# Kernel tuning notes

Hardware: AMD Instinct MI355X
Metric: run time of the kernel (lower is better)

The kernel has to match this reference:

```python
import jax, jax.numpy as jnp
import numpy as np

SCALE = 4
KUP = 5


def conv2d(x, w, b, pad=0):
    # x: (B,C,H,W), w: (O,I,kh,kw)
    y = jax.lax.conv_general_dilated(x, w, (1, 1), [(pad, pad), (pad, pad)],
                                     dimension_numbers=('NCHW', 'OIHW', 'NCHW'))
    return y + b[None, :, None, None]


def unfold(x, k):
    # torch F.unfold equivalent: (B,C,H,W) -> (B,C,k*k,H,W), channel-major patch order
    p = jax.lax.conv_general_dilated_patches(x, (k, k), (1, 1), [(k // 2, k // 2), (k // 2, k // 2)])
    B, _, H, W = p.shape
    return p.reshape(B, -1, k * k, H, W)


def layernorm(x, g, b, eps=1e-5):
    m = jnp.mean(x, -1, keepdims=True)
    v = jnp.mean((x - m) ** 2, -1, keepdims=True)
    return (x - m) * jax.lax.rsqrt(v + eps) * g + b


def sim(q, k):
    # q: (B,sH,sW,E) high-res queries, k: (B,H,W,E) low-res keys
    B, H, W, C = k.shape
    s, ku = SCALE, KUP
    q6 = q.reshape(B, H, s, W, s, C)
    kunf = unfold(jnp.transpose(k, (0, 3, 1, 2)), ku)  # (B,E,ku^2,H,W)
    a = jnp.einsum('bhswtc,bcphw->bhswtp', q6, kunf)
    return a.reshape(B, s * H, s * W, ku * ku)


def atn(attn, x):
    # attn: (B,sH,sW,ku^2), x: (B,H,W,C) low-res values
    B, H, W, C = x.shape
    s, ku = SCALE, KUP
    a6 = attn.reshape(B, H, s, W, s, ku * ku)
    xunf = unfold(jnp.transpose(x, (0, 3, 1, 2)), ku)  # (B,C,ku^2,H,W)
    o = jnp.einsum('bhswtp,bcphw->bhswtc', a6, xunf)
    return o.reshape(B, s * H, s * W, C)


def setup_inputs() -> dict:
    key = jax.random.key(0)
    ks = jax.random.split(key, 40)
    B, C, H, W, yC, E = 2, 64, 128, 128, 3, 64
    sc = 0.05
    def n(i, shape):
        return jax.random.normal(ks[i], shape, jnp.float32) * sc
    return {
        'x': jax.random.normal(ks[0], (B, C, H, W), jnp.float32),
        'y': jax.random.normal(ks[1], (B, yC, H * SCALE, W * SCALE), jnp.float32),
        'gate_w': n(2, (C, C, 1, 1)), 'gate_b': n(3, (C,)),
        'pc1a_w': n(4, (16, yC + C, 1, 1)), 'pc1a_b': n(5, (16,)),
        'pc1b_w': n(6, (16, 16, 5, 5)), 'pc1b_b': n(7, (16,)),
        'spa1_w': n(8, (16, 16, 3, 3)), 'spa1_b': n(9, (16,)),
        'spa2_w': n(10, (16, 16, 3, 3)), 'spa2_b': n(11, (16,)),
        'frq1_w': n(12, (16, 16, 1, 1)), 'frq1_b': n(13, (16,)),
        'frq2_w': n(14, (16, 16, 1, 1)), 'frq2_b': n(15, (16,)),
        'cat_w': n(16, (8, 32, 1, 1)), 'cat_b': n(17, (8,)),
        'ca1_w': n(18, (2, 8, 1, 1)), 'ca1_b': n(19, (2,)),
        'ca2_w': n(20, (8, 2, 1, 1)), 'ca2_b': n(21, (8,)),
        'pc3_w': n(22, (C, 8, 1, 1)), 'pc3_b': n(23, (C,)),
        'lny_g': jnp.ones((C,), jnp.float32), 'lny_b': jnp.zeros((C,), jnp.float32),
        'lnx_g': jnp.ones((C,), jnp.float32), 'lnx_b': jnp.zeros((C,), jnp.float32),
        'q_w': n(24, (E, C)), 'q_b': n(25, (E,)),
        'k_w': n(26, (E, C)), 'k_b': n(27, (E,)),
    }


def reference(x, y, gate_w, gate_b, pc1a_w, pc1a_b, pc1b_w, pc1b_b,
              spa1_w, spa1_b, spa2_w, spa2_b, frq1_w, frq1_b, frq2_w, frq2_b,
              cat_w, cat_b, ca1_w, ca1_b, ca2_w, ca2_b, pc3_w, pc3_b,
              lny_g, lny_b, lnx_g, lnx_b, q_w, q_b, k_w, k_b):
    B, C, H, W = x.shape
    s = SCALE
    up_x = jax.image.resize(x, (B, C, H * s, W * s), 'cubic')
    gate = jax.nn.sigmoid(conv2d(up_x, gate_w, gate_b))
    # pan_conv1: 1x1 then 5x5
    f = conv2d(jnp.concatenate([y, up_x], 1), pc1a_w, pc1a_b)
    f = conv2d(f, pc1b_w, pc1b_b, pad=2)
    # DDNF: spatial branch (residual conv block stand-in) + frequency branch (1x1 stand-in), cat -> 8ch
    spa = f + conv2d(jax.nn.relu(conv2d(f, spa1_w, spa1_b, pad=1)), spa2_w, spa2_b, pad=1)
    frq = conv2d(jax.nn.relu(conv2d(f, frq1_w, frq1_b)), frq2_w, frq2_b)
    f = conv2d(jnp.concatenate([spa, frq], 1), cat_w, cat_b)
    # ChannelAttention(8, reduction=4): SE-style
    pooled = jnp.mean(f, (2, 3), keepdims=True)
    w = jax.nn.sigmoid(conv2d(jax.nn.relu(conv2d(pooled, ca1_w, ca1_b)), ca2_w, ca2_b))
    f = f * w
    enc = conv2d(f, pc3_w, pc3_b)  # (B,C,sH,sW)
    yb = jnp.transpose(enc, (0, 2, 3, 1))
    xb = jnp.transpose(x, (0, 2, 3, 1))
    yn = layernorm(yb, lny_g, lny_b)
    xn = layernorm(xb, lnx_g, lnx_b)
    q = yn @ q_w.T + q_b  # (B,sH,sW,E)
    k = xn @ k_w.T + k_b  # (B,H,W,E)
    attn = jax.nn.softmax(sim(q, k), axis=-1)
    sapa = jnp.transpose(atn(attn, xb), (0, 3, 1, 2))
    final = gate * sapa + (1.0 - gate) * enc
    return (final, sapa, enc)
```

## Files before the change

### kernel.cpp

```cpp
#include <hip/hip_runtime.h>
#include <hip/hip_bf16.h>
#include <math.h>


#define DEVFN static __device__ __forceinline__

DEVFN float keys_w(float d) {
    if (d < 1.f) return ((1.5f * d - 2.5f) * d) * d + 1.f;
    if (d < 2.f) return ((-0.5f * d + 2.5f) * d - 4.f) * d + 2.f;
    return 0.f;
}

DEVFN void bicubic_axis(int o, int n, int idx4[4], float w4[4]) {
    float f = (o + 0.5f) * 0.25f - 0.5f;
    float fb = floorf(f);
    int ib = (int)fb;
    float t = f - fb;
    float ws[4];
    ws[0] = keys_w(1.f + t);
    ws[1] = keys_w(t);
    ws[2] = keys_w(1.f - t);
    ws[3] = keys_w(2.f - t);
    float s = 0.f;
#pragma unroll
    for (int m = 0; m < 4; m++) {
        int ix = ib - 1 + m;
        if (ix < 0 || ix >= n) ws[m] = 0.f;
        s += ws[m];
        idx4[m] = min(max(ix, 0), n - 1);
    }
    float inv = 1.f / s;
#pragma unroll
    for (int m = 0; m < 4; m++) w4[m] = ws[m] * inv;
}

DEVFN float sigm(float v) { return 1.f / (1.f + __expf(-v)); }

DEVFN unsigned short f2bf(float f) {
    __hip_bfloat16 h = __float2bfloat16(f);
    unsigned short u;
    __builtin_memcpy(&u, &h, 2);
    return u;
}
DEVFN float bf2f(unsigned short u) {
    union { unsigned int i; float f; } z;
    z.i = ((unsigned int)u) << 16;
    return z.f;
}

__global__ __launch_bounds__(256) void k_low(const float* __restrict__ x,
                                             const float* __restrict__ gw, const float* __restrict__ gb,
                                             const float* __restrict__ pw,
                                             const float* __restrict__ lg, const float* __restrict__ lb,
                                             const float* __restrict__ kw, const float* __restrict__ kbias,
                                             float* __restrict__ kb, float* __restrict__ xb,
                                             float* __restrict__ glo, float* __restrict__ plo) {
    int idx = blockIdx.x * 256 + threadIdx.x;
    int w = idx & 127, h = (idx >> 7) & 127, b = idx >> 14;
    const float* xp = x + (size_t)b * 64 * 16384 + (h << 7) + w;
    float xv[64];
#pragma unroll
    for (int c = 0; c < 64; c++) xv[c] = xp[(size_t)c << 14];
    float4* xbp = (float4*)(xb + (size_t)idx * 64);
#pragma unroll
    for (int c4 = 0; c4 < 16; c4++)
        xbp[c4] = make_float4(xv[4 * c4], xv[4 * c4 + 1], xv[4 * c4 + 2], xv[4 * c4 + 3]);
    float4* gp = (float4*)(glo + (size_t)idx * 64);
#pragma unroll
    for (int e4 = 0; e4 < 16; e4++) {
        float r[4];
#pragma unroll
        for (int u = 0; u < 4; u++) {
            int e = e4 * 4 + u;
            float s = gb[e];
#pragma unroll
            for (int c = 0; c < 64; c++) s = fmaf(xv[c], gw[e * 64 + c], s);
            r[u] = s;
        }
        gp[e4] = make_float4(r[0], r[1], r[2], r[3]);
    }
    float4* pp = (float4*)(plo + (size_t)idx * 16);
#pragma unroll
    for (int e4 = 0; e4 < 4; e4++) {
        float r[4];
#pragma unroll
        for (int u = 0; u < 4; u++) {
            int e = e4 * 4 + u;
            float s = 0.f;
#pragma unroll
            for (int c = 0; c < 64; c++) s = fmaf(xv[c], pw[e * 67 + 3 + c], s);
            r[u] = s;
        }
        pp[e4] = make_float4(r[0], r[1], r[2], r[3]);
    }
    float m = 0.f;
#pragma unroll
    for (int c = 0; c < 64; c++) m += xv[c];
    m *= (1.f / 64.f);
    float var = 0.f;
#pragma unroll
    for (int c = 0; c < 64; c++) {
        float d = xv[c] - m;
        var = fmaf(d, d, var);
    }
    var *= (1.f / 64.f);
    float rstd = rsqrtf(var + 1e-5f);
#pragma unroll
    for (int c = 0; c < 64; c++) xv[c] = (xv[c] - m) * rstd * lg[c] + lb[c];
    float4* kp = (float4*)(kb + (size_t)idx * 64);
#pragma unroll
    for (int e4 = 0; e4 < 16; e4++) {
        float r[4];
#pragma unroll
        for (int u = 0; u < 4; u++) {
            int e = e4 * 4 + u;
            float s = kbias[e];
#pragma unroll
            for (int c = 0; c < 64; c++) s = fmaf(xv[c], kw[e * 64 + c], s);
            r[u] = s;
        }
        kp[e4] = make_float4(r[0], r[1], r[2], r[3]);
    }
}

__global__ __launch_bounds__(256) void k_gp(const float* __restrict__ glo, const float* __restrict__ plo,
                                            const float* __restrict__ y,
                                            const float* __restrict__ paw, const float* __restrict__ pab,
                                            __hip_bfloat16* __restrict__ gate, float* __restrict__ f0) {
    __shared__ float v[68 * 81];
    int bid = blockIdx.x;
    int b = bid >> 10, i = (bid >> 1) & 511, j0 = (bid & 1) << 8;
    int t = threadIdx.x;
    int iy[4];
    float wy[4];
    bicubic_axis(i, 128, iy, wy);
    int c0 = (j0 >> 2) - 2;
    for (int e = t; e < 68 * 80; e += 256) {
        int ch = e % 80, lc = e / 80;
        int gc = c0 + lc;
        float val = 0.f;
        if ((unsigned)gc < 128u) {
            if (ch < 64) {
                val = wy[0] * glo[(size_t)((b * 128 + iy[0]) * 128 + gc) * 64 + ch] +
                      wy[1] * glo[(size_t)((b * 128 + iy[1]) * 128 + gc) * 64 + ch] +
                      wy[2] * glo[(size_t)((b * 128 + iy[2]) * 128 + gc) * 64 + ch] +
                      wy[3] * glo[(size_t)((b * 128 + iy[3]) * 128 + gc) * 64 + ch];
            } else {
                int cc = ch - 64;
                val = wy[0] * plo[(size_t)((b * 128 + iy[0]) * 128 + gc) * 16 + cc] +
                      wy[1] * plo[(size_t)((b * 128 + iy[1]) * 128 + gc) * 16 + cc] +
                      wy[2] * plo[(size_t)((b * 128 + iy[2]) * 128 + gc) * 16 + cc] +
                      wy[3] * plo[(size_t)((b * 128 + iy[3]) * 128 + gc) * 16 + cc];
            }
        }
        v[lc * 81 + ch] = val;
    }
    __syncthreads();
    int j = j0 + t;
    int jx[4];
    float wx[4];
    bicubic_axis(j, 128, jx, wx);
    int lx0 = jx[0] - c0, lx1 = jx[1] - c0, lx2 = jx[2] - c0, lx3 = jx[3] - c0;
    float out[80];
#pragma unroll
    for (int ch = 0; ch < 80; ch++)
        out[ch] = wx[0] * v[lx0 * 81 + ch] + wx[1] * v[lx1 * 81 + ch] +
                  wx[2] * v[lx2 * 81 + ch] + wx[3] * v[lx3 * 81 + ch];
    size_t pxoff = ((size_t)b << 18) + ((size_t)i << 9) + j;
    unsigned int uu[32];
#pragma unroll
    for (int k = 0; k < 32; k++) {
        unsigned short h0 = f2bf(sigm(out[2 * k]));
        unsigned short h1 = f2bf(sigm(out[2 * k + 1]));
        uu[k] = (unsigned int)h0 | ((unsigned int)h1 << 16);
    }
    uint4* gp4 = (uint4*)((unsigned short*)gate + pxoff * 64);
#pragma unroll
    for (int k4 = 0; k4 < 8; k4++)
        gp4[k4] = make_uint4(uu[4 * k4], uu[4 * k4 + 1], uu[4 * k4 + 2], uu[4 * k4 + 3]);
    float yc0 = y[((size_t)(b * 3 + 0) << 18) + ((size_t)i << 9) + j];
    float yc1 = y[((size_t)(b * 3 + 1) << 18) + ((size_t)i << 9) + j];
    float yc2 = y[((size_t)(b * 3 + 2) << 18) + ((size_t)i << 9) + j];
    float4* fp = (float4*)(f0 + pxoff * 16);
#pragma unroll
    for (int e4 = 0; e4 < 4; e4++) {
        float r[4];
#pragma unroll
        for (int u = 0; u < 4; u++) {
            int oc = e4 * 4 + u;
            r[u] = out[64 + oc] + pab[oc] + yc0 * paw[oc * 67 + 0] + yc1 * paw[oc * 67 + 1] + yc2 * paw[oc * 67 + 2];
        }
        fp[e4] = make_float4(r[0], r[1], r[2], r[3]);
    }
}

__global__ __launch_bounds__(256) void k_conv5(const float* __restrict__ fin,
                                               const float* __restrict__ w,
                                               const float* __restrict__ bias,
                                               float* __restrict__ fout) {
    int idx = blockIdx.x * 256 + threadIdx.x;
    int j = idx & 511, i = (idx >> 9) & 511, b = idx >> 18;
    float acc[16];
#pragma unroll
    for (int oc = 0; oc < 16; oc++) acc[oc] = bias[oc];
    for (int ky = 0; ky < 5; ky++) {
        int iy = i + ky - 2;
        if ((unsigned)iy >= 512u) continue;
        for (int kx = 0; kx < 5; kx++) {
            int jx = j + kx - 2;
            if ((unsigned)jx >= 512u) continue;
            const float4* fp = (const float4*)(fin + (((size_t)b << 18) + ((size_t)iy << 9) + jx) * 16);
            float vv[16];
            *(float4*)(vv + 0) = fp[0];
            *(float4*)(vv + 4) = fp[1];
            *(float4*)(vv + 8) = fp[2];
            *(float4*)(vv + 12) = fp[3];
            int kidx = ky * 5 + kx;
#pragma unroll
            for (int ic = 0; ic < 16; ic++) {
#pragma unroll
                for (int oc = 0; oc < 16; oc++)
                    acc[oc] = fmaf(vv[ic], w[(oc * 16 + ic) * 25 + kidx], acc[oc]);
            }
        }
    }
    float4* op = (float4*)(fout + (size_t)idx * 16);
#pragma unroll
    for (int e4 = 0; e4 < 4; e4++)
        op[e4] = make_float4(acc[4 * e4], acc[4 * e4 + 1], acc[4 * e4 + 2], acc[4 * e4 + 3]);
}

__global__ __launch_bounds__(256) void k_conv3r(const float* __restrict__ fin,
                                                const float* __restrict__ w,
                                                const float* __restrict__ bias,
                                                float* __restrict__ fout) {
    int idx = blockIdx.x * 256 + threadIdx.x;
    int j = idx & 511, i = (idx >> 9) & 511, b = idx >> 18;
    float acc[16];
#pragma unroll
    for (int oc = 0; oc < 16; oc++) acc[oc] = bias[oc];
#pragma unroll
    for (int ky = 0; ky < 3; ky++) {
        int iy = i + ky - 1;
        if ((unsigned)iy >= 512u) continue;
#pragma unroll
        for (int kx = 0; kx < 3; kx++) {
            int jx = j + kx - 1;
            if ((unsigned)jx >= 512u) continue;
            const float4* fp = (const float4*)(fin + (((size_t)b << 18) + ((size_t)iy << 9) + jx) * 16);
            float vv[16];
            *(float4*)(vv + 0) = fp[0];
            *(float4*)(vv + 4) = fp[1];
            *(float4*)(vv + 8) = fp[2];
            *(float4*)(vv + 12) = fp[3];
            int kidx = ky * 3 + kx;
#pragma unroll
            for (int ic = 0; ic < 16; ic++) {
#pragma unroll
                for (int oc = 0; oc < 16; oc++)
                    acc[oc] = fmaf(vv[ic], w[(oc * 16 + ic) * 9 + kidx], acc[oc]);
            }
        }
    }
    float4* op = (float4*)(fout + (size_t)idx * 16);
#pragma unroll
    for (int e4 = 0; e4 < 4; e4++)
        op[e4] = make_float4(fmaxf(acc[4 * e4], 0.f), fmaxf(acc[4 * e4 + 1], 0.f),
                             fmaxf(acc[4 * e4 + 2], 0.f), fmaxf(acc[4 * e4 + 3], 0.f));
}

__global__ __launch_bounds__(256) void k_tail(const float* __restrict__ f1,
                                              const float* __restrict__ t,
                                              const float* __restrict__ s2w, const float* __restrict__ s2b,
                                              const float* __restrict__ q1w, const float* __restrict__ q1b,
                                              const float* __restrict__ q2w, const float* __restrict__ q2b,
                                              const float* __restrict__ cw_, const float* __restrict__ cb_,
                                              float* __restrict__ f8) {
    int idx = blockIdx.x * 256 + threadIdx.x;
    int j = idx & 511, i = (idx >> 9) & 511, b = idx >> 18;
    float sp[16];
#pragma unroll
    for (int oc = 0; oc < 16; oc++) sp[oc] = s2b[oc];
#pragma unroll
    for (int ky = 0; ky < 3; ky++) {
        int iy = i + ky - 1;
        if ((unsigned)iy >= 512u) continue;
#pragma unroll
        for (int kx = 0; kx < 3; kx++) {
            int jx = j + kx - 1;
            if ((unsigned)jx >= 512u) continue;
            const float4* fp = (const float4*)(t + (((size_t)b << 18) + ((size_t)iy << 9) + jx) * 16);
            float vv[16];
            *(float4*)(vv + 0) = fp[0];
            *(float4*)(vv + 4) = fp[1];
            *(float4*)(vv + 8) = fp[2];
            *(float4*)(vv + 12) = fp[3];
            int kidx = ky * 3 + kx;
#pragma unroll
            for (int ic = 0; ic < 16; ic++) {
#pragma unroll
                for (int oc = 0; oc < 16; oc++)
                    sp[oc] = fmaf(vv[ic], s2w[(oc * 16 + ic) * 9 + kidx], sp[oc]);
            }
        }
    }
    float fv[16];
    const float4* f1p = (const float4*)(f1 + (size_t)idx * 16);
    *(float4*)(fv + 0) = f1p[0];
    *(float4*)(fv + 4) = f1p[1];
    *(float4*)(fv + 8) = f1p[2];
    *(float4*)(fv + 12) = f1p[3];
#pragma unroll
    for (int c = 0; c < 16; c++) sp[c] += fv[c];
    float mid[16];
#pragma unroll
    for (int r = 0; r < 16; r++) {
        float m = q1b[r];
#pragma unroll
        for (int c = 0; c < 16; c++) m = fmaf(fv[c], q1w[r * 16 + c], m);
        mid[r] = fmaxf(m, 0.f);
    }
    float fo[16];
#pragma unroll
    for (int r = 0; r < 16; r++) {
        float m = q2b[r];
#pragma unroll
        for (int c = 0; c < 16; c++) m = fmaf(mid[c], q2w[r * 16 + c], m);
        fo[r] = m;
    }
    float r8[8];
#pragma unroll
    for (int o = 0; o < 8; o++) {
        float a = cb_[o];
#pragma unroll
        for (int c = 0; c < 16; c++) a = fmaf(sp[c], cw_[o * 32 + c], a);
#pragma unroll
        for (int c = 0; c < 16; c++) a = fmaf(fo[c], cw_[o * 32 + 16 + c], a);
        r8[o] = a;
    }
    float4* op = (float4*)(f8 + (size_t)idx * 8);
    op[0] = make_float4(r8[0], r8[1], r8[2], r8[3]);
    op[1] = make_float4(r8[4], r8[5], r8[6], r8[7]);
}

__global__ __launch_bounds__(256) void k_pool(const float* __restrict__ f8, float* __restrict__ partials) {
    int b = blockIdx.x >> 4, blk = blockIdx.x & 15;
    const float4* fp = (const float4*)(f8 + (((size_t)b) << 18) * 8);
    float acc[8];
#pragma unroll
    for (int c = 0; c < 8; c++) acc[c] = 0.f;
    int p0 = blk * 16384;
    for (int p = p0 + threadIdx.x; p < p0 + 16384; p += 256) {
        float4 a0 = fp[p * 2], a1 = fp[p * 2 + 1];
        acc[0] += a0.x; acc[1] += a0.y; acc[2] += a0.z; acc[3] += a0.w;
        acc[4] += a1.x; acc[5] += a1.y; acc[6] += a1.z; acc[7] += a1.w;
    }
#pragma unroll
    for (int off = 32; off; off >>= 1) {
#pragma unroll
        for (int c = 0; c < 8; c++) acc[c] += __shfl_down(acc[c], off, 64);
    }
    __shared__ float ls[4][8];
    int lane = threadIdx.x & 63, wv = threadIdx.x >> 6;
    if (lane == 0) {
#pragma unroll
        for (int c = 0; c < 8; c++) ls[wv][c] = acc[c];
    }
    __syncthreads();
    if (threadIdx.x < 8) {
        float s = ls[0][threadIdx.x] + ls[1][threadIdx.x] + ls[2][threadIdx.x] + ls[3][threadIdx.x];
        partials[(b * 8 + threadIdx.x) * 16 + blk] = s;
    }
}

__global__ void k_se(const float* __restrict__ partials,
                     const float* __restrict__ w1, const float* __restrict__ b1,
                     const float* __restrict__ w2, const float* __restrict__ b2,
                     float* __restrict__ cw) {
    int b = threadIdx.x;
    if (b >= 2) return;
    float pooled[8];
#pragma unroll
    for (int c = 0; c < 8; c++) {
        float s = 0.f;
#pragma unroll
        for (int k = 0; k < 16; k++) s += partials[(b * 8 + c) * 16 + k];
        pooled[c] = s * (1.f / 262144.f);
    }
    float mid[2];
#pragma unroll
    for (int r = 0; r < 2; r++) {
        float m = b1[r];
#pragma unroll
        for (int c = 0; c < 8; c++) m = fmaf(w1[r * 8 + c], pooled[c], m);
        mid[r] = fmaxf(m, 0.f);
    }
#pragma unroll
    for (int c = 0; c < 8; c++) {
        float v = b2[c] + w2[c * 2 + 0] * mid[0] + w2[c * 2 + 1] * mid[1];
        cw[b * 8 + c] = 1.f / (1.f + __expf(-v));
    }
}

__global__ __launch_bounds__(256) void k_pc3(const float* __restrict__ f8, const float* __restrict__ cw,
                                             const float* __restrict__ w, const float* __restrict__ bias,
                                             const float* __restrict__ lg, const float* __restrict__ lb,
                                             const float* __restrict__ qw, const float* __restrict__ qbias,
                                             float* __restrict__ enc, unsigned short* __restrict__ qbuf) {
    int idx = blockIdx.x * 256 + threadIdx.x;
    int b = idx >> 18;
    size_t hi = (size_t)idx & 262143;
    const float4* fp = (const float4*)(f8 + (size_t)idx * 8);
    float4 a0 = fp[0], a1 = fp[1];
    float v[8] = {a0.x, a0.y, a0.z, a0.w, a1.x, a1.y, a1.z, a1.w};
#pragma unroll
    for (int c = 0; c < 8; c++) v[c] *= cw[b * 8 + c];
    float yn[64];
#pragma unroll
    for (int oc = 0; oc < 64; oc++) {
        float a = bias[oc];
#pragma unroll
        for (int c = 0; c < 8; c++) a = fmaf(v[c], w[oc * 8 + c], a);
        yn[oc] = a;
        enc[((size_t)(b * 64 + oc) << 18) + hi] = a;
    }
    float m = 0.f;
#pragma unroll
    for (int c = 0; c < 64; c++) m += yn[c];
    m *= (1.f / 64.f);
    float var = 0.f;
#pragma unroll
    for (int c = 0; c < 64; c++) {
        float d = yn[c] - m;
        var = fmaf(d, d, var);
    }
    var *= (1.f / 64.f);
    float rstd = rsqrtf(var + 1e-5f);
#pragma unroll
    for (int c = 0; c < 64; c++) yn[c] = (yn[c] - m) * rstd * lg[c] + lb[c];
    unsigned short* qp = qbuf + (size_t)idx * 64;
    for (int e0 = 0; e0 < 64; e0 += 8) {
        float qv[8];
#pragma unroll
        for (int u = 0; u < 8; u++) {
            float s = qbias[e0 + u];
#pragma unroll
            for (int c = 0; c < 64; c++) s = fmaf(yn[c], qw[(e0 + u) * 64 + c], s);
            qv[u] = s;
        }
        unsigned int pk[4];
#pragma unroll
        for (int u = 0; u < 4; u++)
            pk[u] = (unsigned int)f2bf(qv[2 * u]) | ((unsigned int)f2bf(qv[2 * u + 1]) << 16);
        *(uint4*)(qp + e0) = make_uint4(pk[0], pk[1], pk[2], pk[3]);
    }
}

__global__ __launch_bounds__(256) void k_attn(const float* __restrict__ enc,
                                              const __hip_bfloat16* __restrict__ gate,
                                              const unsigned short* __restrict__ qb,
                                              const float* __restrict__ kb, const float* __restrict__ xbv,
                                              float* __restrict__ sapa, float* __restrict__ fin) {
    __shared__ float tile[100 * 68];
    int tid = threadIdx.x;
    int bid = blockIdx.x;
    int b = bid >> 12, i = (bid >> 3) & 511, jb = bid & 7;
    int j0 = jb << 6;
    int h = i >> 2;
    int wbase = j0 >> 2;
    int cg = tid & 3, px = tid >> 2;
    int j = j0 + px;
    size_t pix = ((size_t)b << 18) + ((size_t)i << 9) + j;
    const uint4* qp = (const uint4*)(qb + pix * 64 + cg * 16);
    uint4 q0 = qp[0], q1 = qp[1];
    unsigned int qu[8] = {q0.x, q0.y, q0.z, q0.w, q1.x, q1.y, q1.z, q1.w};
    float q[16];
#pragma unroll
    for (int k = 0; k < 8; k++) {
        q[2 * k] = bf2f((unsigned short)(qu[k] & 0xffff));
        q[2 * k + 1] = bf2f((unsigned short)(qu[k] >> 16));
    }
    for (int s = tid; s < 1600; s += 256) {
        int p = s >> 4, e4 = s & 15;
        int row = p / 20, col = p - row * 20;
        int hh = h - 2 + row, ww = wbase - 2 + col;
        float4 val = make_float4(0.f, 0.f, 0.f, 0.f);
        if ((unsigned)hh < 128u && (unsigned)ww < 128u)
            val = ((const float4*)(kb + (size_t)((b * 128 + hh) * 128 + ww) * 64))[e4];
        *(float4*)(tile + p * 68 + e4 * 4) = val;
    }
    __syncthreads();
    int wl = px >> 2;
    float a[25];
#pragma unroll
    for (int dy = 0; dy < 5; dy++) {
#pragma unroll
        for (int dx = 0; dx < 5; dx++) {
            int lp = dy * 20 + wl + dx;
            const float4* kp = (const float4*)(tile + lp * 68 + cg * 16);
            float s = 0.f;
#pragma unroll
            for (int e4 = 0; e4 < 4; e4++) {
                float4 kv = kp[e4];
                s = fmaf(q[4 * e4 + 0], kv.x, s);
                s = fmaf(q[4 * e4 + 1], kv.y, s);
                s = fmaf(q[4 * e4 + 2], kv.z, s);
                s = fmaf(q[4 * e4 + 3], kv.w, s);
            }
            a[dy * 5 + dx] = s;
        }
    }
#pragma unroll
    for (int p = 0; p < 25; p++) {
        a[p] += __shfl_xor(a[p], 1, 4);
        a[p] += __shfl_xor(a[p], 2, 4);
    }
    float mx = a[0];
#pragma unroll
    for (int p = 1; p < 25; p++) mx = fmaxf(mx, a[p]);
    float Z = 0.f;
#pragma unroll
    for (int p = 0; p < 25; p++) {
        a[p] = __expf(a[p] - mx);
        Z += a[p];
    }
    float invZ = 1.f / Z;
    __syncthreads();
    for (int s = tid; s < 1600; s += 256) {
        int p = s >> 4, e4 = s & 15;
        int row = p / 20, col = p - row * 20;
        int hh = h - 2 + row, ww = wbase - 2 + col;
        float4 val = make_float4(0.f, 0.f, 0.f, 0.f);
        if ((unsigned)hh < 128u && (unsigned)ww < 128u)
            val = ((const float4*)(xbv + (size_t)((b * 128 + hh) * 128 + ww) * 64))[e4];
        *(float4*)(tile + p * 68 + e4 * 4) = val;
    }
    __syncthreads();
    float o[16];
#pragma unroll
    for (int k = 0; k < 16; k++) o[k] = 0.f;
#pragma unroll
    for (int dy = 0; dy < 5; dy++) {
#pragma unroll
        for (int dx = 0; dx < 5; dx++) {
            float wp = a[dy * 5 + dx];
            int lp = dy * 20 + wl + dx;
            const float4* xp = (const float4*)(tile + lp * 68 + cg * 16);
#pragma unroll
            for (int e4 = 0; e4 < 4; e4++) {
                float4 xv = xp[e4];
                o[4 * e4 + 0] = fmaf(wp, xv.x, o[4 * e4 + 0]);
                o[4 * e4 + 1] = fmaf(wp, xv.y, o[4 * e4 + 1]);
                o[4 * e4 + 2] = fmaf(wp, xv.z, o[4 * e4 + 2]);
                o[4 * e4 + 3] = fmaf(wp, xv.w, o[4 * e4 + 3]);
            }
        }
    }
    const uint4* gp4 = (const uint4*)((const unsigned short*)gate + pix * 64 + cg * 16);
    uint4 g0 = gp4[0], g1 = gp4[1];
    unsigned int gu[8] = {g0.x, g0.y, g0.z, g0.w, g1.x, g1.y, g1.z, g1.w};
    size_t obase = ((size_t)b << 24) + ((size_t)i << 9) + j;
    const float* ep = enc + obase;
#pragma unroll
    for (int cc = 0; cc < 16; cc++) {
        int c = cg * 16 + cc;
        size_t oidx = obase + ((size_t)c << 18);
        float sv = o[cc] * invZ;
        sapa[oidx] = sv;
        unsigned int wbits = gu[cc >> 1];
        unsigned short hb = (cc & 1) ? (unsigned short)(wbits >> 16) : (unsigned short)(wbits & 0xffff);
        float gv = bf2f(hb);
        float ev = ep[(size_t)c << 18];
        fin[oidx] = gv * sv + (1.f - gv) * ev;
    }
}

extern "C" void kernel_launch(void* const* d_in, const int* in_sizes, int n_in,
                              void* d_out, int out_size, void* d_ws, size_t ws_size,
                              hipStream_t stream) {
    const float* x = (const float*)d_in[0];
    const float* y = (const float*)d_in[1];
    const float* gate_w = (const float*)d_in[2];
    const float* gate_b = (const float*)d_in[3];
    const float* pc1a_w = (const float*)d_in[4];
    const float* pc1a_b = (const float*)d_in[5];
    const float* pc1b_w = (const float*)d_in[6];
    const float* pc1b_b = (const float*)d_in[7];
    const float* spa1_w = (const float*)d_in[8];
    const float* spa1_b = (const float*)d_in[9];
    const float* spa2_w = (const float*)d_in[10];
    const float* spa2_b = (const float*)d_in[11];
    const float* frq1_w = (const float*)d_in[12];
    const float* frq1_b = (const float*)d_in[13];
    const float* frq2_w = (const float*)d_in[14];
    const float* frq2_b = (const float*)d_in[15];
    const float* cat_w = (const float*)d_in[16];
    const float* cat_b = (const float*)d_in[17];
    const float* ca1_w = (const float*)d_in[18];
    const float* ca1_b = (const float*)d_in[19];
    const float* ca2_w = (const float*)d_in[20];
    const float* ca2_b = (const float*)d_in[21];
    const float* pc3_w = (const float*)d_in[22];
    const float* pc3_b = (const float*)d_in[23];
    const float* lny_g = (const float*)d_in[24];
    const float* lny_b = (const float*)d_in[25];
    const float* lnx_g = (const float*)d_in[26];
    const float* lnx_b = (const float*)d_in[27];
    const float* q_w = (const float*)d_in[28];
    const float* q_b = (const float*)d_in[29];
    const float* k_w = (const float*)d_in[30];
    const float* k_b = (const float*)d_in[31];

    float* out = (float*)d_out;
    float* finalp = out;
    float* sapap = out + 33554432;
    float* encp = out + 67108864;

    char* ws = (char*)d_ws;
    __hip_bfloat16* gate = (__hip_bfloat16*)ws;
    float* f0 = (float*)(ws + 67108864);
    float* f1 = (float*)(ws + 100663296);
    float* f8 = (float*)(ws + 134217728);
    float* kbuf = (float*)(ws + 150994944);
    float* xbuf = (float*)(ws + 159383552);
    float* partials = (float*)(ws + 167772160);
    float* cw = (float*)(ws + 167773184);
    float* glo = f1;
    float* plo = f1 + 2097152;
    float* tbuf = f0;
    unsigned short* qbuf = (unsigned short*)(ws + 67108864);

    dim3 blk(256);
    dim3 gridHi(2048);

    k_low<<<dim3(128), blk, 0, stream>>>(x, gate_w, gate_b, pc1a_w, lnx_g, lnx_b, k_w, k_b,
                                         kbuf, xbuf, glo, plo);
    k_gp<<<gridHi, blk, 0, stream>>>(glo, plo, y, pc1a_w, pc1a_b, gate, f0);
    k_conv5<<<gridHi, blk, 0, stream>>>(f0, pc1b_w, pc1b_b, f1);
    k_conv3r<<<gridHi, blk, 0, stream>>>(f1, spa1_w, spa1_b, tbuf);
    k_tail<<<gridHi, blk, 0, stream>>>(f1, tbuf, spa2_w, spa2_b, frq1_w, frq1_b,
                                       frq2_w, frq2_b, cat_w, cat_b, f8);
    k_pool<<<dim3(32), blk, 0, stream>>>(f8, partials);
    k_se<<<dim3(1), dim3(64), 0, stream>>>(partials, ca1_w, ca1_b, ca2_w, ca2_b, cw);
    k_pc3<<<gridHi, blk, 0, stream>>>(f8, cw, pc3_w, pc3_b, lny_g, lny_b, q_w, q_b, encp, qbuf);
    k_attn<<<dim3(8192), blk, 0, stream>>>(encp, gate, qbuf, kbuf, xbuf, sapap, finalp);
}
```

Before: 946.5 us.

## Reuse conv input rows across wavefront lanes via shuffles in stencil kernels

The 5x5, 3x3 and tail conv kernels now assign each 64-lane wavefront a 60-column row segment. Each lane loads one 16-channel pixel per filter row, and the remaining horizontal taps are obtained from neighbour lanes with shuffles instead of separate global loads. This cuts redundant global/L1 loads by roughly the kernel width, at the cost of many shuffle instructions and a few idle halo lanes. Launch grids are resized to cover 9 segments per row.

Result: slower. 1.270 ms (+34.2%).

```diff
diff --git a/kernel.cpp b/kernel.cpp
--- a/kernel.cpp
+++ b/kernel.cpp
@@ -198,75 +198,118 @@
                                                const float* __restrict__ w,
                                                const float* __restrict__ bias,
                                                float* __restrict__ fout) {
-    int idx = blockIdx.x * 256 + threadIdx.x;
-    int j = idx & 511, i = (idx >> 9) & 511, b = idx >> 18;
+    int W = blockIdx.x * 4 + (threadIdx.x >> 6);
+    int lane = threadIdx.x & 63;
+    int seg = W % 9;
+    int rw = W / 9;
+    int i = rw & 511, b = rw >> 9;
+    int j0 = seg * 60;
+    int colL = j0 + lane - 2;
+    bool colOK = (unsigned)colL < 512u;
     float acc[16];
 #pragma unroll
     for (int oc = 0; oc < 16; oc++) acc[oc] = bias[oc];
     for (int ky = 0; ky < 5; ky++) {
         int iy = i + ky - 2;
-        if ((unsigned)iy >= 512u) continue;
-        for (int kx = 0; kx < 5; kx++) {
-            int jx = j + kx - 2;
-            if ((unsigned)jx >= 512u) continue;
-            const float4* fp = (const float4*)(fin + (((size_t)b << 18) + ((size_t)iy << 9) + jx) * 16);
-            float vv[16];
-            *(float4*)(vv + 0) = fp[0];
-            *(float4*)(vv + 4) = fp[1];
-            *(float4*)(vv + 8) = fp[2];
-            *(float4*)(vv + 12) = fp[3];
-            int kidx = ky * 5 + kx;
+        float t0[16];
+        if ((unsigned)iy < 512u && colOK) {
+            const float4* p = (const float4*)(fin + (((size_t)b << 18) + ((size_t)iy << 9) + colL) * 16);
+            *(float4*)(t0 + 0) = p[0];
+            *(float4*)(t0 + 4) = p[1];
+            *(float4*)(t0 + 8) = p[2];
+            *(float4*)(t0 + 12) = p[3];
+        } else {
+#pragma unroll
+            for (int ic = 0; ic < 16; ic++) t0[ic] = 0.f;
+        }
+#pragma unroll
+        for (int ic = 0; ic < 16; ic++) {
+            float v = t0[ic];
+#pragma unroll
+            for (int oc = 0; oc < 16; oc++)
+                acc[oc] = fmaf(v, w[(oc * 16 + ic) * 25 + ky * 5 + 0], acc[oc]);
+        }
+#pragma unroll
+        for (int dx = 1; dx < 5; dx++) {
+            float tv[16];
+#pragma unroll
+            for (int ic = 0; ic < 16; ic++) tv[ic] = __shfl(t0[ic], lane + dx, 64);
 #pragma unroll
             for (int ic = 0; ic < 16; ic++) {
+                float v = tv[ic];
 #pragma unroll
                 for (int oc = 0; oc < 16; oc++)
-                    acc[oc] = fmaf(vv[ic], w[(oc * 16 + ic) * 25 + kidx], acc[oc]);
+                    acc[oc] = fmaf(v, w[(oc * 16 + ic) * 25 + ky * 5 + dx], acc[oc]);
             }
         }
     }
-    float4* op = (float4*)(fout + (size_t)idx * 16);
-#pragma unroll
-    for (int e4 = 0; e4 < 4; e4++)
-        op[e4] = make_float4(acc[4 * e4], acc[4 * e4 + 1], acc[4 * e4 + 2], acc[4 * e4 + 3]);
+    int j = j0 + lane;
+    if (lane < 60 && j < 512) {
+        float4* op = (float4*)(fout + (((size_t)b << 18) + ((size_t)i << 9) + j) * 16);
+        op[0] = make_float4(acc[0], acc[1], acc[2], acc[3]);
+        op[1] = make_float4(acc[4], acc[5], acc[6], acc[7]);
+        op[2] = make_float4(acc[8], acc[9], acc[10], acc[11]);
+        op[3] = make_float4(acc[12], acc[13], acc[14], acc[15]);
+    }
 }
 
 __global__ __launch_bounds__(256) void k_conv3r(const float* __restrict__ fin,
                                                 const float* __restrict__ w,
                                                 const float* __restrict__ bias,
                                                 float* __restrict__ fout) {
-    int idx = blockIdx.x * 256 + threadIdx.x;
-    int j = idx & 511, i = (idx >> 9) & 511, b = idx >> 18;
+    int W = blockIdx.x * 4 + (threadIdx.x >> 6);
+    int lane = threadIdx.x & 63;
+    int seg = W % 9;
+    int rw = W / 9;
+    int i = rw & 511, b = rw >> 9;
+    int j0 = seg * 60;
+    int colL = j0 + lane - 1;
+    bool colOK = (unsigned)colL < 512u;
     float acc[16];
 #pragma unroll
     for (int oc = 0; oc < 16; oc++) acc[oc] = bias[oc];
-#pragma unroll
     for (int ky = 0; ky < 3; ky++) {
         int iy = i + ky - 1;
-        if ((unsigned)iy >= 512u) continue;
-#pragma unroll
-        for (int kx = 0; kx < 3; kx++) {
-            int jx = j + kx - 1;
-            if ((unsigned)jx >= 512u) continue;
-            const float4* fp = (const float4*)(fin + (((size_t)b << 18) + ((size_t)iy << 9) + jx) * 16);
-            float vv[16];
-            *(float4*)(vv + 0) = fp[0];
-            *(float4*)(vv + 4) = fp[1];
-            *(float4*)(vv + 8) = fp[2];
-            *(float4*)(vv + 12) = fp[3];
-            int kidx = ky * 3 + kx;
+        float t0[16];
+        if ((unsigned)iy < 512u && colOK) {
+            const float4* p = (const float4*)(fin + (((size_t)b << 18) + ((size_t)iy << 9) + colL) * 16);
+            *(float4*)(t0 + 0) = p[0];
+            *(float4*)(t0 + 4) = p[1];
+            *(float4*)(t0 + 8) = p[2];
+            *(float4*)(t0 + 12) = p[3];
+        } else {
+#pragma unroll
+            for (int ic = 0; ic < 16; ic++) t0[ic] = 0.f;
+        }
+#pragma unroll
+        for (int ic = 0; ic < 16; ic++) {
+            float v = t0[ic];
+#pragma unroll
+            for (int oc = 0; oc < 16; oc++)
+                acc[oc] = fmaf(v, w[(oc * 16 + ic) * 9 + ky * 3 + 0], acc[oc]);
+        }
+#pragma unroll
+        for (int dx = 1; dx < 3; dx++) {
+            float tv[16];
+#pragma unroll
+            for (int ic = 0; ic < 16; ic++) tv[ic] = __shfl(t0[ic], lane + dx, 64);
 #pragma unroll
             for (int ic = 0; ic < 16; ic++) {
+                float v = tv[ic];
 #pragma unroll
                 for (int oc = 0; oc < 16; oc++)
-                    acc[oc] = fmaf(vv[ic], w[(oc * 16 + ic) * 9 + kidx], acc[oc]);
+                    acc[oc] = fmaf(v, w[(oc * 16 + ic) * 9 + ky * 3 + dx], acc[oc]);
             }
         }
     }
-    float4* op = (float4*)(fout + (size_t)idx * 16);
-#pragma unroll
-    for (int e4 = 0; e4 < 4; e4++)
-        op[e4] = make_float4(fmaxf(acc[4 * e4], 0.f), fmaxf(acc[4 * e4 + 1], 0.f),
-                             fmaxf(acc[4 * e4 + 2], 0.f), fmaxf(acc[4 * e4 + 3], 0.f));
+    int j = j0 + lane;
+    if (lane < 60 && j < 512) {
+        float4* op = (float4*)(fout + (((size_t)b << 18) + ((size_t)i << 9) + j) * 16);
+        op[0] = make_float4(fmaxf(acc[0], 0.f), fmaxf(acc[1], 0.f), fmaxf(acc[2], 0.f), fmaxf(acc[3], 0.f));
+        op[1] = make_float4(fmaxf(acc[4], 0.f), fmaxf(acc[5], 0.f), fmaxf(acc[6], 0.f), fmaxf(acc[7], 0.f));
+        op[2] = make_float4(fmaxf(acc[8], 0.f), fmaxf(acc[9], 0.f), fmaxf(acc[10], 0.f), fmaxf(acc[11], 0.f));
+        op[3] = make_float4(fmaxf(acc[12], 0.f), fmaxf(acc[13], 0.f), fmaxf(acc[14], 0.f), fmaxf(acc[15], 0.f));
+    }
 }
 
 __global__ __launch_bounds__(256) void k_tail(const float* __restrict__ f1,
@@ -276,40 +319,64 @@
                                               const float* __restrict__ q2w, const float* __restrict__ q2b,
                                               const float* __restrict__ cw_, const float* __restrict__ cb_,
                                               float* __restrict__ f8) {
-    int idx = blockIdx.x * 256 + threadIdx.x;
-    int j = idx & 511, i = (idx >> 9) & 511, b = idx >> 18;
+    int W = blockIdx.x * 4 + (threadIdx.x >> 6);
+    int lane = threadIdx.x & 63;
+    int seg = W % 9;
+    int rw = W / 9;
+    int i = rw & 511, b = rw >> 9;
+    int j0 = seg * 60;
+    int colL = j0 + lane - 1;
+    bool colOK = (unsigned)colL < 512u;
+    int j = j0 + lane;
+    bool outOK = (lane < 60) && (j < 512);
     float sp[16];
 #pragma unroll
     for (int oc = 0; oc < 16; oc++) sp[oc] = s2b[oc];
-#pragma unroll
     for (int ky = 0; ky < 3; ky++) {
         int iy = i + ky - 1;
-        if ((unsigned)iy >= 512u) continue;
-#pragma unroll
-        for (int kx = 0; kx < 3; kx++) {
-            int jx = j + kx - 1;
-            if ((unsigned)jx >= 512u) continue;
-            const float4* fp = (const float4*)(t + (((size_t)b << 18) + ((size_t)iy << 9) + jx) * 16);
-            float vv[16];
-            *(float4*)(vv + 0) = fp[0];
-            *(float4*)(vv + 4) = fp[1];
-            *(float4*)(vv + 8) = fp[2];
-            *(float4*)(vv + 12) = fp[3];
-            int kidx = ky * 3 + kx;
+        float t0[16];
+        if ((unsigned)iy < 512u && colOK) {
+            const float4* p = (const float4*)(t + (((size_t)b << 18) + ((size_t)iy << 9) + colL) * 16);
+            *(float4*)(t0 + 0) = p[0];
+            *(float4*)(t0 + 4) = p[1];
+            *(float4*)(t0 + 8) = p[2];
+            *(float4*)(t0 + 12) = p[3];
+        } else {
+#pragma unroll
+            for (int ic = 0; ic < 16; ic++) t0[ic] = 0.f;
+        }
+#pragma unroll
+        for (int ic = 0; ic < 16; ic++) {
+            float v = t0[ic];
+#pragma unroll
+            for (int oc = 0; oc < 16; oc++)
+                sp[oc] = fmaf(v, s2w[(oc * 16 + ic) * 9 + ky * 3 + 0], sp[oc]);
+        }
+#pragma unroll
+        for (int dx = 1; dx < 3; dx++) {
+            float tv[16];
+#pragma unroll
+            for (int ic = 0; ic < 16; ic++) tv[ic] = __shfl(t0[ic], lane + dx, 64);
 #pragma unroll
             for (int ic = 0; ic < 16; ic++) {
+                float v = tv[ic];
 #pragma unroll
                 for (int oc = 0; oc < 16; oc++)
-                    sp[oc] = fmaf(vv[ic], s2w[(oc * 16 + ic) * 9 + kidx], sp[oc]);
+                    sp[oc] = fmaf(v, s2w[(oc * 16 + ic) * 9 + ky * 3 + dx], sp[oc]);
             }
         }
     }
     float fv[16];
-    const float4* f1p = (const float4*)(f1 + (size_t)idx * 16);
-    *(float4*)(fv + 0) = f1p[0];
-    *(float4*)(fv + 4) = f1p[1];
-    *(float4*)(fv + 8) = f1p[2];
-    *(float4*)(fv + 12) = f1p[3];
+    if (outOK) {
+        const float4* f1p = (const float4*)(f1 + (((size_t)b << 18) + ((size_t)i << 9) + j) * 16);
+        *(float4*)(fv + 0) = f1p[0];
+        *(float4*)(fv + 4) = f1p[1];
+        *(float4*)(fv + 8) = f1p[2];
+        *(float4*)(fv + 12) = f1p[3];
+    } else {
+#pragma unroll
+        for (int c = 0; c < 16; c++) fv[c] = 0.f;
+    }
 #pragma unroll
     for (int c = 0; c < 16; c++) sp[c] += fv[c];
     float mid[16];
@@ -338,9 +405,11 @@
         for (int c = 0; c < 16; c++) a = fmaf(fo[c], cw_[o * 32 + 16 + c], a);
         r8[o] = a;
     }
-    float4* op = (float4*)(f8 + (size_t)idx * 8);
-    op[0] = make_float4(r8[0], r8[1], r8[2], r8[3]);
-    op[1] = make_float4(r8[4], r8[5], r8[6], r8[7]);
+    if (outOK) {
+        float4* op = (float4*)(f8 + (((size_t)b << 18) + ((size_t)i << 9) + j) * 8);
+        op[0] = make_float4(r8[0], r8[1], r8[2], r8[3]);
+        op[1] = make_float4(r8[4], r8[5], r8[6], r8[7]);
+    }
 }
 
 __global__ __launch_bounds__(256) void k_pool(const float* __restrict__ f8, float* __restrict__ partials) {
@@ -632,14 +701,15 @@
 
     dim3 blk(256);
     dim3 gridHi(2048);
+    dim3 gridWave(2304);
 
     k_low<<<dim3(128), blk, 0, stream>>>(x, gate_w, gate_b, pc1a_w, lnx_g, lnx_b, k_w, k_b,
                                          kbuf, xbuf, glo, plo);
     k_gp<<<gridHi, blk, 0, stream>>>(glo, plo, y, pc1a_w, pc1a_b, gate, f0);
-    k_conv5<<<gridHi, blk, 0, stream>>>(f0, pc1b_w, pc1b_b, f1);
-    k_conv3r<<<gridHi, blk, 0, stream>>>(f1, spa1_w, spa1_b, tbuf);
-    k_tail<<<gridHi, blk, 0, stream>>>(f1, tbuf, spa2_w, spa2_b, frq1_w, frq1_b,
-                                       frq2_w, frq2_b, cat_w, cat_b, f8);
+    k_conv5<<<gridWave, blk, 0, stream>>>(f0, pc1b_w, pc1b_b, f1);
+    k_conv3r<<<gridWave, blk, 0, stream>>>(f1, spa1_w, spa1_b, tbuf);
+    k_tail<<<gridWave, blk, 0, stream>>>(f1, tbuf, spa2_w, spa2_b, frq1_w, frq1_b,
+                                         frq2_w, frq2_b, cat_w, cat_b, f8);
     k_pool<<<dim3(32), blk, 0, stream>>>(f8, partials);
     k_se<<<dim3(1), dim3(64), 0, stream>>>(partials, ca1_w, ca1_b, ca2_w, ca2_b, cw);
     k_pc3<<<gridHi, blk, 0, stream>>>(f8, cw, pc3_w, pc3_b, lny_g, lny_b, q_w, q_b, encp, qbuf);
```

## Stage conv input halos in LDS and pre-transpose conv weights

Applied to the files above, without the earlier changes.

The 5x5 and 3x3 high-res convolution kernels now load a 4x64-pixel tile plus halo into shared memory once per block (padded stride of 20 floats per pixel), then read neighbour taps from LDS instead of global memory. A small prep kernel transposes the conv weights to tap-major, oc-contiguous layout so the inner FMA loop reads weights contiguously (uniform scalar loads). Boundary checks move into the tile fill. This adds an extra launch and LDS pressure that could lower occupancy.

After: 846.7 us. 10.5% less time.

```diff
diff --git a/kernel.cpp b/kernel.cpp
--- a/kernel.cpp
+++ b/kernel.cpp
@@ -46,6 +46,24 @@
     union { unsigned int i; float f; } z;
     z.i = ((unsigned int)u) << 16;
     return z.f;
+}
+
+__global__ __launch_bounds__(256) void k_prep(const float* __restrict__ w5,
+                                              const float* __restrict__ w3a,
+                                              const float* __restrict__ w3b,
+                                              float* __restrict__ wT5,
+                                              float* __restrict__ wT3a,
+                                              float* __restrict__ wT3b) {
+    int t = blockIdx.x * 256 + threadIdx.x;
+    if (t < 6400) {
+        int tap = t >> 8, ic = (t >> 4) & 15, oc = t & 15;
+        wT5[t] = w5[(oc * 16 + ic) * 25 + tap];
+    }
+    if (t < 2304) {
+        int tap = t >> 8, ic = (t >> 4) & 15, oc = t & 15;
+        wT3a[t] = w3a[(oc * 16 + ic) * 9 + tap];
+        wT3b[t] = w3b[(oc * 16 + ic) * 9 + tap];
+    }
 }
 
 __global__ __launch_bounds__(256) void k_low(const float* __restrict__ x,
@@ -195,117 +213,157 @@
 }
 
 __global__ __launch_bounds__(256) void k_conv5(const float* __restrict__ fin,
-                                               const float* __restrict__ w,
+                                               const float* __restrict__ wT,
                                                const float* __restrict__ bias,
                                                float* __restrict__ fout) {
-    int idx = blockIdx.x * 256 + threadIdx.x;
-    int j = idx & 511, i = (idx >> 9) & 511, b = idx >> 18;
+    __shared__ float lds[8 * 68 * 20];
+    int tid = threadIdx.x;
+    int bid = blockIdx.x;
+    int seg = bid & 7, it = (bid >> 3) & 127, b = bid >> 10;
+    int i0 = it * 4, j0 = seg * 64;
+    for (int s = tid; s < 2176; s += 256) {
+        int part = s & 3, px = s >> 2;
+        int row = px / 68, col = px - row * 68;
+        int gi = i0 - 2 + row, gj = j0 - 2 + col;
+        float4 v = make_float4(0.f, 0.f, 0.f, 0.f);
+        if ((unsigned)gi < 512u && (unsigned)gj < 512u)
+            v = *(const float4*)(fin + (((size_t)b << 18) + ((size_t)gi << 9) + gj) * 16 + part * 4);
+        *(float4*)(&lds[(row * 68 + col) * 20 + part * 4]) = v;
+    }
+    __syncthreads();
+    int tx = tid & 63, ty = tid >> 6;
     float acc[16];
 #pragma unroll
     for (int oc = 0; oc < 16; oc++) acc[oc] = bias[oc];
+#pragma unroll
     for (int ky = 0; ky < 5; ky++) {
-        int iy = i + ky - 2;
-        if ((unsigned)iy >= 512u) continue;
+#pragma unroll
         for (int kx = 0; kx < 5; kx++) {
-            int jx = j + kx - 2;
-            if ((unsigned)jx >= 512u) continue;
-            const float4* fp = (const float4*)(fin + (((size_t)b << 18) + ((size_t)iy << 9) + jx) * 16);
+            const float* p = &lds[((ty + ky) * 68 + tx + kx) * 20];
             float vv[16];
-            *(float4*)(vv + 0) = fp[0];
-            *(float4*)(vv + 4) = fp[1];
-            *(float4*)(vv + 8) = fp[2];
-            *(float4*)(vv + 12) = fp[3];
-            int kidx = ky * 5 + kx;
+            *(float4*)(vv + 0) = *(const float4*)(p + 0);
+            *(float4*)(vv + 4) = *(const float4*)(p + 4);
+            *(float4*)(vv + 8) = *(const float4*)(p + 8);
+            *(float4*)(vv + 12) = *(const float4*)(p + 12);
+            const float* wp = wT + (ky * 5 + kx) * 256;
 #pragma unroll
             for (int ic = 0; ic < 16; ic++) {
+                float v = vv[ic];
 #pragma unroll
                 for (int oc = 0; oc < 16; oc++)
-                    acc[oc] = fmaf(vv[ic], w[(oc * 16 + ic) * 25 + kidx], acc[oc]);
+                    acc[oc] = fmaf(v, wp[ic * 16 + oc], acc[oc]);
             }
         }
     }
-    float4* op = (float4*)(fout + (size_t)idx * 16);
-#pragma unroll
-    for (int e4 = 0; e4 < 4; e4++)
-        op[e4] = make_float4(acc[4 * e4], acc[4 * e4 + 1], acc[4 * e4 + 2], acc[4 * e4 + 3]);
+    int i = i0 + ty, j = j0 + tx;
+    float4* op = (float4*)(fout + (((size_t)b << 18) + ((size_t)i << 9) + j) * 16);
+    op[0] = make_float4(acc[0], acc[1], acc[2], acc[3]);
+    op[1] = make_float4(acc[4], acc[5], acc[6], acc[7]);
+    op[2] = make_float4(acc[8], acc[9], acc[10], acc[11]);
+    op[3] = make_float4(acc[12], acc[13], acc[14], acc[15]);
 }
 
 __global__ __launch_bounds__(256) void k_conv3r(const float* __restrict__ fin,
-                                                const float* __restrict__ w,
+                                                const float* __restrict__ wT,
                                                 const float* __restrict__ bias,
                                                 float* __restrict__ fout) {
-    int idx = blockIdx.x * 256 + threadIdx.x;
-    int j = idx & 511, i = (idx >> 9) & 511, b = idx >> 18;
+    __shared__ float lds[6 * 66 * 20];
+    int tid = threadIdx.x;
+    int bid = blockIdx.x;
+    int seg = bid & 7, it = (bid >> 3) & 127, b = bid >> 10;
+    int i0 = it * 4, j0 = seg * 64;
+    for (int s = tid; s < 1584; s += 256) {
+        int part = s & 3, px = s >> 2;
+        int row = px / 66, col = px - row * 66;
+        int gi = i0 - 1 + row, gj = j0 - 1 + col;
+        float4 v = make_float4(0.f, 0.f, 0.f, 0.f);
+        if ((unsigned)gi < 512u && (unsigned)gj < 512u)
+            v = *(const float4*)(fin + (((size_t)b << 18) + ((size_t)gi << 9) + gj) * 16 + part * 4);
+        *(float4*)(&lds[(row * 66 + col) * 20 + part * 4]) = v;
+    }
+    __syncthreads();
+    int tx = tid & 63, ty = tid >> 6;
     float acc[16];
 #pragma unroll
     for (int oc = 0; oc < 16; oc++) acc[oc] = bias[oc];
 #pragma unroll
     for (int ky = 0; ky < 3; ky++) {
-        int iy = i + ky - 1;
-        if ((unsigned)iy >= 512u) continue;
 #pragma unroll
         for (int kx = 0; kx < 3; kx++) {
-            int jx = j + kx - 1;
-            if ((unsigned)jx >= 512u) continue;
-            const float4* fp = (const float4*)(fin + (((size_t)b << 18) + ((size_t)iy << 9) + jx) * 16);
+            const float* p = &lds[((ty + ky) * 66 + tx + kx) * 20];
             float vv[16];
-            *(float4*)(vv + 0) = fp[0];
-            *(float4*)(vv + 4) = fp[1];
-            *(float4*)(vv + 8) = fp[2];
-            *(float4*)(vv + 12) = fp[3];
-            int kidx = ky * 3 + kx;
+            *(float4*)(vv + 0) = *(const float4*)(p + 0);
+            *(float4*)(vv + 4) = *(const float4*)(p + 4);
+            *(float4*)(vv + 8) = *(const float4*)(p + 8);
+            *(float4*)(vv + 12) = *(const float4*)(p + 12);
+            const float* wp = wT + (ky * 3 + kx) * 256;
 #pragma unroll
             for (int ic = 0; ic < 16; ic++) {
+                float v = vv[ic];
 #pragma unroll
                 for (int oc = 0; oc < 16; oc++)
-                    acc[oc] = fmaf(vv[ic], w[(oc * 16 + ic) * 9 + kidx], acc[oc]);
+                    acc[oc] = fmaf(v, wp[ic * 16 + oc], acc[oc]);
             }
         }
     }
-    float4* op = (float4*)(fout + (size_t)idx * 16);
-#pragma unroll
-    for (int e4 = 0; e4 < 4; e4++)
-        op[e4] = make_float4(fmaxf(acc[4 * e4], 0.f), fmaxf(acc[4 * e4 + 1], 0.f),
-                             fmaxf(acc[4 * e4 + 2], 0.f), fmaxf(acc[4 * e4 + 3], 0.f));
+    int i = i0 + ty, j = j0 + tx;
+    float4* op = (float4*)(fout + (((size_t)b << 18) + ((size_t)i << 9) + j) * 16);
+    op[0] = make_float4(fmaxf(acc[0], 0.f), fmaxf(acc[1], 0.f), fmaxf(acc[2], 0.f), fmaxf(acc[3], 0.f));
+    op[1] = make_float4(fmaxf(acc[4], 0.f), fmaxf(acc[5], 0.f), fmaxf(acc[6], 0.f), fmaxf(acc[7], 0.f));
+    op[2] = make_float4(fmaxf(acc[8], 0.f), fmaxf(acc[9], 0.f), fmaxf(acc[10], 0.f), fmaxf(acc[11], 0.f));
+    op[3] = make_float4(fmaxf(acc[12], 0.f), fmaxf(acc[13], 0.f), fmaxf(acc[14], 0.f), fmaxf(acc[15], 0.f));
 }
 
 __global__ __launch_bounds__(256) void k_tail(const float* __restrict__ f1,
                                               const float* __restrict__ t,
-                                              const float* __restrict__ s2w, const float* __restrict__ s2b,
+                                              const float* __restrict__ wT2,
+                                              const float* __restrict__ s2b,
                                               const float* __restrict__ q1w, const float* __restrict__ q1b,
                                               const float* __restrict__ q2w, const float* __restrict__ q2b,
                                               const float* __restrict__ cw_, const float* __restrict__ cb_,
                                               float* __restrict__ f8) {
-    int idx = blockIdx.x * 256 + threadIdx.x;
-    int j = idx & 511, i = (idx >> 9) & 511, b = idx >> 18;
+    __shared__ float lds[6 * 66 * 20];
+    int tid = threadIdx.x;
+    int bid = blockIdx.x;
+    int seg = bid & 7, it = (bid >> 3) & 127, b = bid >> 10;
+    int i0 = it * 4, j0 = seg * 64;
+    for (int s = tid; s < 1584; s += 256) {
+        int part = s & 3, px = s >> 2;
+        int row = px / 66, col = px - row * 66;
+        int gi = i0 - 1 + row, gj = j0 - 1 + col;
+        float4 v = make_float4(0.f, 0.f, 0.f, 0.f);
+        if ((unsigned)gi < 512u && (unsigned)gj < 512u)
+            v = *(const float4*)(t + (((size_t)b << 18) + ((size_t)gi << 9) + gj) * 16 + part * 4);
+        *(float4*)(&lds[(row * 66 + col) * 20 + part * 4]) = v;
+    }
+    __syncthreads();
+    int tx = tid & 63, ty = tid >> 6;
+    int i = i0 + ty, j = j0 + tx;
     float sp[16];
 #pragma unroll
     for (int oc = 0; oc < 16; oc++) sp[oc] = s2b[oc];
 #pragma unroll
     for (int ky = 0; ky < 3; ky++) {
-        int iy = i + ky - 1;
-        if ((unsigned)iy >= 512u) continue;
 #pragma unroll
         for (int kx = 0; kx < 3; kx++) {
-            int jx = j + kx - 1;
-            if ((unsigned)jx >= 512u) continue;
-            const float4* fp = (const float4*)(t + (((size_t)b << 18) + ((size_t)iy << 9) + jx) * 16);
+            const float* p = &lds[((ty + ky) * 66 + tx + kx) * 20];
             float vv[16];
-            *(float4*)(vv + 0) = fp[0];
-            *(float4*)(vv + 4) = fp[1];
-            *(float4*)(vv + 8) = fp[2];
-            *(float4*)(vv + 12) = fp[3];
-            int kidx = ky * 3 + kx;
+            *(float4*)(vv + 0) = *(const float4*)(p + 0);
+            *(float4*)(vv + 4) = *(const float4*)(p + 4);
+            *(float4*)(vv + 8) = *(const float4*)(p + 8);
+            *(float4*)(vv + 12) = *(const float4*)(p + 12);
+            const float* wp = wT2 + (ky * 3 + kx) * 256;
 #pragma unroll
             for (int ic = 0; ic < 16; ic++) {
+                float v = vv[ic];
 #pragma unroll
                 for (int oc = 0; oc < 16; oc++)
-                    sp[oc] = fmaf(vv[ic], s2w[(oc * 16 + ic) * 9 + kidx], sp[oc]);
+                    sp[oc] = fmaf(v, wp[ic * 16 + oc], sp[oc]);
             }
         }
     }
     float fv[16];
-    const float4* f1p = (const float4*)(f1 + (size_t)idx * 16);
+    const float4* f1p = (const float4*)(f1 + (((size_t)b << 18) + ((size_t)i << 9) + j) * 16);
     *(float4*)(fv + 0) = f1p[0];
     *(float4*)(fv + 4) = f1p[1];
     *(float4*)(fv + 8) = f1p[2];
@@ -338,7 +396,7 @@
         for (int c = 0; c < 16; c++) a = fmaf(fo[c], cw_[o * 32 + 16 + c], a);
         r8[o] = a;
     }
-    float4* op = (float4*)(f8 + (size_t)idx * 8);
+    float4* op = (float4*)(f8 + (((size_t)b << 18) + ((size_t)i << 9) + j) * 8);
     op[0] = make_float4(r8[0], r8[1], r8[2], r8[3]);
     op[1] = make_float4(r8[4], r8[5], r8[6], r8[7]);
 }
@@ -625,6 +683,9 @@
     float* xbuf = (float*)(ws + 159383552);
     float* partials = (float*)(ws + 167772160);
     float* cw = (float*)(ws + 167773184);
+    float* wT5 = (float*)(ws + 167773248);
+    float* wT3a = (float*)(ws + 167798848);
+    float* wT3b = (float*)(ws + 167808064);
     float* glo = f1;
     float* plo = f1 + 2097152;
     float* tbuf = f0;
@@ -632,14 +693,16 @@
 
     dim3 blk(256);
     dim3 gridHi(2048);
-
+    dim3 gridConv(2048);
+
+    k_prep<<<dim3(25), blk, 0, stream>>>(pc1b_w, spa1_w, spa2_w, wT5, wT3a, wT3b);
     k_low<<<dim3(128), blk, 0, stream>>>(x, gate_w, gate_b, pc1a_w, lnx_g, lnx_b, k_w, k_b,
                                          kbuf, xbuf, glo, plo);
     k_gp<<<gridHi, blk, 0, stream>>>(glo, plo, y, pc1a_w, pc1a_b, gate, f0);
-    k_conv5<<<gridHi, blk, 0, stream>>>(f0, pc1b_w, pc1b_b, f1);
-    k_conv3r<<<gridHi, blk, 0, stream>>>(f1, spa1_w, spa1_b, tbuf);
-    k_tail<<<gridHi, blk, 0, stream>>>(f1, tbuf, spa2_w, spa2_b, frq1_w, frq1_b,
-                                       frq2_w, frq2_b, cat_w, cat_b, f8);
+    k_conv5<<<gridConv, blk, 0, stream>>>(f0, wT5, pc1b_b, f1);
+    k_conv3r<<<gridConv, blk, 0, stream>>>(f1, wT3a, spa1_b, tbuf);
+    k_tail<<<gridConv, blk, 0, stream>>>(f1, tbuf, wT3b, spa2_b, frq1_w, frq1_b,
+                                         frq2_w, frq2_b, cat_w, cat_b, f8);
     k_pool<<<dim3(32), blk, 0, stream>>>(f8, partials);
     k_se<<<dim3(1), dim3(64), 0, stream>>>(partials, ca1_w, ca1_b, ca2_w, ca2_b, cw);
     k_pc3<<<gridHi, blk, 0, stream>>>(f8, cw, pc3_w, pc3_b, lny_g, lny_b, q_w, q_b, encp, qbuf);
```
